# Optimization experiments

Measured on AMD Instinct MI355X. Metric: run time of the kernel, lower is better.

The kernel has to match this reference:

```python
import jax, jax.numpy as jnp
import numpy as np

E = 800_000      # number of edges
D = 256          # d_model_edge
N = 50_000       # number of atoms/nodes


def setup_inputs() -> dict:
    key = jax.random.key(0)
    k1, k2, k3, k4, k5 = jax.random.split(key, 5)
    forces = jax.random.normal(k1, (E, D), dtype=jnp.float32)
    V_st = jax.random.normal(k2, (E, 3), dtype=jnp.float32)
    # MLP([D, D, 1]): Linear(D,D) + act + Linear(D,1). Scaled init for stability.
    W1 = jax.random.normal(k3, (D, D), dtype=jnp.float32) * (1.0 / np.sqrt(D))
    b1 = jnp.zeros((D,), dtype=jnp.float32)
    W2 = jax.random.normal(k4, (D, 1), dtype=jnp.float32) * (1.0 / np.sqrt(D))
    b2 = jnp.zeros((1,), dtype=jnp.float32)
    idx_t = jax.random.randint(k5, (E,), 0, N, dtype=jnp.int64 if jax.config.jax_enable_x64 else jnp.int32)
    return {
        "forces": forces,
        "V_st": V_st,
        "W1": W1,
        "b1": b1,
        "W2": W2,
        "b2": b2,
        "idx_t": idx_t,
        "n_atoms": N,
    }


def reference(forces, V_st, W1, b1, W2, b2, idx_t, n_atoms):
    # out_mlp: Linear(D,D) -> SiLU -> Linear(D,1)
    h = jax.nn.silu(forces @ W1 + b1)          # [E, D]
    s = h @ W2 + b2                            # [E, 1] per-edge scalar
    ev = s * V_st                              # [E, 3] scaled direction vectors
    # scatter-sum over target node indices (reduction='sum')
    out = jax.ops.segment_sum(ev, idx_t, num_segments=n_atoms)  # [N, 3]
    return out
```

## Files before the change

### kernel.cpp

```cpp
#include <hip/hip_runtime.h>
#include <hip/hip_bf16.h>

typedef __attribute__((ext_vector_type(8))) short short8;
typedef __attribute__((ext_vector_type(4))) float floatx4;
typedef unsigned short u16;

#define D 256
#define BM 32
#define NT 128

__device__ __forceinline__ short f2bf(float f) {
    return __builtin_bit_cast(short, __float2bfloat16(f));
}

__global__ void prep_kernel(const float* __restrict__ W1, u16* __restrict__ W1F,
                            float* __restrict__ out, int outn) {
    const int b = blockIdx.x;
    if (b < D) {
        const int k = b, n = threadIdx.x;
        const int k0t = k >> 5, g = (k >> 3) & 3, j = k & 7;
        const int nt = n >> 4, l15 = n & 15;
        W1F[(long)((((k0t << 4) + nt) << 6) + (g << 4) + l15) * 8 + j] = (u16)f2bf(W1[k * D + n]);
    } else {
        int i = (b - D) * 256 + threadIdx.x;
        const int stride = (gridDim.x - D) * 256;
        for (; i < outn; i += stride) out[i] = 0.f;
    }
}

struct R8 { floatx4 f0, f1; };

__launch_bounds__(NT, 4)
__global__ void head_kernel(const float* __restrict__ forces,
                            const float* __restrict__ V_st,
                            const u16*   __restrict__ W1F,
                            const float* __restrict__ b1,
                            const float* __restrict__ W2,
                            const float* __restrict__ b2,
                            const int*   __restrict__ idx_t,
                            float* __restrict__ out,
                            int E) {
    __shared__ u16 Albs[16 * 512];
    __shared__ float s_red[2][BM];

    const int tid  = threadIdx.x;
    const int lane = tid & 63;
    const int wn   = tid >> 6;
    const int l15  = lane & 15;
    const int g    = lane >> 4;

    const long row0 = (long)blockIdx.x * BM;

    float vx = 0.f, vy = 0.f, vz = 0.f;
    int node = -1;
    if (tid < BM) {
        long e = row0 + tid;
        vx = V_st[e * 3 + 0]; vy = V_st[e * 3 + 1]; vz = V_st[e * 3 + 2];
        node = idx_t[e];
    }

    const int arow = tid >> 2;
    const int agg  = tid & 3;
    const float* abase = forces + (row0 + arow) * D + agg * 8;

    R8 r[8];
#pragma unroll
    for (int k0t = 0; k0t < 8; ++k0t) {
        r[k0t].f0 = *(const floatx4*)(abase + k0t * 32);
        r[k0t].f1 = *(const floatx4*)(abase + k0t * 32 + 4);
    }
    const int aslot = ((agg << 4) | (arow & 15)) * 8;
    const int art   = arow >> 4;
#pragma unroll
    for (int k0t = 0; k0t < 8; ++k0t) {
        short8 a;
#pragma unroll
        for (int j = 0; j < 4; ++j) { a[j] = f2bf(r[k0t].f0[j]); a[4 + j] = f2bf(r[k0t].f1[j]); }
        *(short8*)&Albs[(k0t * 2 + art) * 512 + aslot] = a;
    }
    __syncthreads();

    floatx4 acc[2][8];
#pragma unroll
    for (int mr = 0; mr < 2; ++mr)
#pragma unroll
        for (int nc = 0; nc < 8; ++nc)
            acc[mr][nc] = (floatx4){0.f, 0.f, 0.f, 0.f};

#pragma unroll
    for (int k0t = 0; k0t < 8; ++k0t) {
        short8 bf[8], af[2];
#pragma unroll
        for (int nc = 0; nc < 8; ++nc)
            bf[nc] = *(const short8*)(W1F + (long)((k0t * 16 + wn * 8 + nc) * 64 + lane) * 8);
#pragma unroll
        for (int mr = 0; mr < 2; ++mr)
            af[mr] = *(const short8*)&Albs[(k0t * 2 + mr) * 512 + lane * 8];
#pragma unroll
        for (int mr = 0; mr < 2; ++mr)
#pragma unroll
            for (int nc = 0; nc < 8; ++nc)
                acc[mr][nc] = __builtin_amdgcn_mfma_f32_16x16x32_bf16(
                    af[mr], bf[nc], acc[mr][nc], 0, 0, 0);
    }

    float b1v[8], w2v[8];
#pragma unroll
    for (int nc = 0; nc < 8; ++nc) {
        int n = wn * 128 + nc * 16 + l15;
        b1v[nc] = b1[n];
        w2v[nc] = W2[n];
    }
    float part[2][4];
#pragma unroll
    for (int mr = 0; mr < 2; ++mr)
#pragma unroll
        for (int rr = 0; rr < 4; ++rr) {
            float sv = 0.f;
#pragma unroll
            for (int nc = 0; nc < 8; ++nc) {
                float z = acc[mr][nc][rr] + b1v[nc];
                float h = z / (1.f + __expf(-z));
                sv += h * w2v[nc];
            }
            part[mr][rr] = sv;
        }

#pragma unroll
    for (int off = 1; off < 16; off <<= 1)
#pragma unroll
        for (int mr = 0; mr < 2; ++mr)
#pragma unroll
            for (int rr = 0; rr < 4; ++rr)
                part[mr][rr] += __shfl_xor(part[mr][rr], off, 16);

    if (l15 == 0) {
#pragma unroll
        for (int mr = 0; mr < 2; ++mr)
#pragma unroll
            for (int rr = 0; rr < 4; ++rr)
                s_red[wn][mr * 16 + g * 4 + rr] = part[mr][rr];
    }
    __syncthreads();

    if (node >= 0) {
        float sv = s_red[0][tid] + s_red[1][tid] + b2[0];
        atomicAdd(&out[(long)node * 3 + 0], sv * vx);
        atomicAdd(&out[(long)node * 3 + 1], sv * vy);
        atomicAdd(&out[(long)node * 3 + 2], sv * vz);
    }
}

extern "C" void kernel_launch(void* const* d_in, const int* in_sizes, int n_in,
                              void* d_out, int out_size, void* d_ws, size_t ws_size,
                              hipStream_t stream) {
    const float* forces = (const float*)d_in[0];
    const float* V_st   = (const float*)d_in[1];
    const float* W1     = (const float*)d_in[2];
    const float* b1     = (const float*)d_in[3];
    const float* W2     = (const float*)d_in[4];
    const float* b2     = (const float*)d_in[5];
    const int*   idx    = (const int*)d_in[6];
    const int E = in_sizes[6];

    u16* W1F = (u16*)d_ws;

    prep_kernel<<<D + 128, 256, 0, stream>>>(W1, W1F, (float*)d_out, out_size);
    const int grid = E / BM;
    head_kernel<<<grid, NT, 0, stream>>>(forces, V_st, W1F, b1, W2, b2, idx,
                                         (float*)d_out, E);
}
```

Before: 291.3 us.

## Warp-specialize head kernel into persistent producer/consumer with double-buffered LDS

Replaces the one-tile-per-block launch with 512 persistent blocks of 512 threads. Four producer waves load and convert the next 64-row forces tile into a second LDS buffer while four consumer waves run MFMA, SiLU and the W2 reduction on the current tile. The aim is to overlap global-memory streaming of forces with the matrix compute and to cut per-block launch overhead. In exchange, half the waves do no math, a block-wide barrier runs every iteration, and occupancy depends on the larger LDS footprint and the 512-thread launch bounds.

```diff
diff --git a/kernel.cpp b/kernel.cpp
--- a/kernel.cpp
+++ b/kernel.cpp
@@ -6,8 +6,9 @@
 typedef unsigned short u16;
 
 #define D 256
-#define BM 32
-#define NT 128
+#define BM 64
+#define NT 512
+#define NBLK 512
 
 __device__ __forceinline__ short f2bf(float f) {
     return __builtin_bit_cast(short, __float2bfloat16(f));
@@ -28,8 +29,6 @@
     }
 }
 
-struct R8 { floatx4 f0, f1; };
-
 __launch_bounds__(NT, 4)
 __global__ void head_kernel(const float* __restrict__ forces,
                             const float* __restrict__ V_st,
@@ -40,114 +39,121 @@
                             const int*   __restrict__ idx_t,
                             float* __restrict__ out,
                             int E) {
-    __shared__ u16 Albs[16 * 512];
-    __shared__ float s_red[2][BM];
+    __shared__ u16 Abuf[2][32 * 512];
+    __shared__ float s_red[2][2][BM];
 
     const int tid  = threadIdx.x;
     const int lane = tid & 63;
-    const int wn   = tid >> 6;
-    const int l15  = lane & 15;
-    const int g    = lane >> 4;
+    const int w    = tid >> 6;
+    const int ntiles = E / BM;
+    const long b = blockIdx.x;
+    const int niter = (int)((ntiles - b + NBLK - 1) / NBLK);
 
-    const long row0 = (long)blockIdx.x * BM;
+    const int arow  = tid >> 2;
+    const int agg   = tid & 3;
+    const int art   = arow >> 4;
+    const int aslot = ((agg << 4) | (arow & 15)) * 8;
+
+    auto FILL = [&](int buf, long tile) {
+        const float* abase = forces + (tile * BM + arow) * (long)D + agg * 8;
+        floatx4 f0[8], f1[8];
+#pragma unroll
+        for (int k0t = 0; k0t < 8; ++k0t) {
+            f0[k0t] = *(const floatx4*)(abase + k0t * 32);
+            f1[k0t] = *(const floatx4*)(abase + k0t * 32 + 4);
+        }
+#pragma unroll
+        for (int k0t = 0; k0t < 8; ++k0t) {
+            short8 a;
+#pragma unroll
+            for (int j = 0; j < 4; ++j) { a[j] = f2bf(f0[k0t][j]); a[4 + j] = f2bf(f1[k0t][j]); }
+            *(short8*)&Abuf[buf][(k0t * 4 + art) * 512 + aslot] = a;
+        }
+    };
+
+    const int cw  = w - 4;
+    const int wm  = (cw >> 1) & 1;
+    const int wn  = cw & 1;
+    const int l15 = lane & 15;
+    const int g   = lane >> 4;
+
+    if (w < 4) FILL(0, b);
+    __syncthreads();
 
     float vx = 0.f, vy = 0.f, vz = 0.f;
-    int node = -1;
-    if (tid < BM) {
-        long e = row0 + tid;
-        vx = V_st[e * 3 + 0]; vy = V_st[e * 3 + 1]; vz = V_st[e * 3 + 2];
-        node = idx_t[e];
-    }
+    int nd = 0;
 
-    const int arow = tid >> 2;
-    const int agg  = tid & 3;
-    const float* abase = forces + (row0 + arow) * D + agg * 8;
+    for (int i = 0; i < niter; ++i) {
+        const int cur = i & 1;
+        const long t = b + (long)i * NBLK;
 
-    R8 r[8];
+        if (w < 4) {
+            if (i + 1 < niter) FILL(cur ^ 1, t + NBLK);
+        } else {
+            if (w == 4) {
+                long e = t * BM + lane;
+                vx = V_st[e * 3 + 0]; vy = V_st[e * 3 + 1]; vz = V_st[e * 3 + 2];
+                nd = idx_t[e];
+            }
+            floatx4 acc[2][8];
 #pragma unroll
-    for (int k0t = 0; k0t < 8; ++k0t) {
-        r[k0t].f0 = *(const floatx4*)(abase + k0t * 32);
-        r[k0t].f1 = *(const floatx4*)(abase + k0t * 32 + 4);
-    }
-    const int aslot = ((agg << 4) | (arow & 15)) * 8;
-    const int art   = arow >> 4;
+            for (int mr = 0; mr < 2; ++mr)
 #pragma unroll
-    for (int k0t = 0; k0t < 8; ++k0t) {
-        short8 a;
-#pragma unroll
-        for (int j = 0; j < 4; ++j) { a[j] = f2bf(r[k0t].f0[j]); a[4 + j] = f2bf(r[k0t].f1[j]); }
-        *(short8*)&Albs[(k0t * 2 + art) * 512 + aslot] = a;
-    }
-    __syncthreads();
-
-    floatx4 acc[2][8];
-#pragma unroll
-    for (int mr = 0; mr < 2; ++mr)
-#pragma unroll
-        for (int nc = 0; nc < 8; ++nc)
-            acc[mr][nc] = (floatx4){0.f, 0.f, 0.f, 0.f};
+                for (int nc = 0; nc < 8; ++nc)
+                    acc[mr][nc] = (floatx4){0.f, 0.f, 0.f, 0.f};
 
 #pragma unroll
-    for (int k0t = 0; k0t < 8; ++k0t) {
-        short8 bf[8], af[2];
+            for (int k0t = 0; k0t < 8; ++k0t) {
+                short8 af0 = *(const short8*)&Abuf[cur][(k0t * 4 + wm * 2 + 0) * 512 + lane * 8];
+                short8 af1 = *(const short8*)&Abuf[cur][(k0t * 4 + wm * 2 + 1) * 512 + lane * 8];
 #pragma unroll
-        for (int nc = 0; nc < 8; ++nc)
-            bf[nc] = *(const short8*)(W1F + (long)((k0t * 16 + wn * 8 + nc) * 64 + lane) * 8);
+                for (int nc = 0; nc < 8; ++nc) {
+                    short8 bf = *(const short8*)(W1F +
+                        (long)((k0t * 16 + wn * 8 + nc) * 64 + lane) * 8);
+                    acc[0][nc] = __builtin_amdgcn_mfma_f32_16x16x32_bf16(af0, bf, acc[0][nc], 0, 0, 0);
+                    acc[1][nc] = __builtin_amdgcn_mfma_f32_16x16x32_bf16(af1, bf, acc[1][nc], 0, 0, 0);
+                }
+            }
+
+            float part[2][4];
 #pragma unroll
-        for (int mr = 0; mr < 2; ++mr)
-            af[mr] = *(const short8*)&Albs[(k0t * 2 + mr) * 512 + lane * 8];
+            for (int mr = 0; mr < 2; ++mr)
 #pragma unroll
-        for (int mr = 0; mr < 2; ++mr)
+                for (int rr = 0; rr < 4; ++rr) {
+                    float sv = 0.f;
 #pragma unroll
-            for (int nc = 0; nc < 8; ++nc)
-                acc[mr][nc] = __builtin_amdgcn_mfma_f32_16x16x32_bf16(
-                    af[mr], bf[nc], acc[mr][nc], 0, 0, 0);
-    }
-
-    float b1v[8], w2v[8];
+                    for (int nc = 0; nc < 8; ++nc) {
+                        int n = wn * 128 + nc * 16 + l15;
+                        float z = acc[mr][nc][rr] + b1[n];
+                        float h = z / (1.f + __expf(-z));
+                        sv += h * W2[n];
+                    }
+                    part[mr][rr] = sv;
+                }
 #pragma unroll
-    for (int nc = 0; nc < 8; ++nc) {
-        int n = wn * 128 + nc * 16 + l15;
-        b1v[nc] = b1[n];
-        w2v[nc] = W2[n];
-    }
-    float part[2][4];
+            for (int off = 1; off < 16; off <<= 1)
 #pragma unroll
-    for (int mr = 0; mr < 2; ++mr)
+                for (int mr = 0; mr < 2; ++mr)
 #pragma unroll
-        for (int rr = 0; rr < 4; ++rr) {
-            float sv = 0.f;
+                    for (int rr = 0; rr < 4; ++rr)
+                        part[mr][rr] += __shfl_xor(part[mr][rr], off, 16);
+            if (l15 == 0) {
 #pragma unroll
-            for (int nc = 0; nc < 8; ++nc) {
-                float z = acc[mr][nc][rr] + b1v[nc];
-                float h = z / (1.f + __expf(-z));
-                sv += h * w2v[nc];
+                for (int mr = 0; mr < 2; ++mr)
+#pragma unroll
+                    for (int rr = 0; rr < 4; ++rr)
+                        s_red[cur][wn][wm * 32 + mr * 16 + g * 4 + rr] = part[mr][rr];
             }
-            part[mr][rr] = sv;
         }
 
-#pragma unroll
-    for (int off = 1; off < 16; off <<= 1)
-#pragma unroll
-        for (int mr = 0; mr < 2; ++mr)
-#pragma unroll
-            for (int rr = 0; rr < 4; ++rr)
-                part[mr][rr] += __shfl_xor(part[mr][rr], off, 16);
+        __syncthreads();
 
-    if (l15 == 0) {
-#pragma unroll
-        for (int mr = 0; mr < 2; ++mr)
-#pragma unroll
-            for (int rr = 0; rr < 4; ++rr)
-                s_red[wn][mr * 16 + g * 4 + rr] = part[mr][rr];
-    }
-    __syncthreads();
-
-    if (node >= 0) {
-        float sv = s_red[0][tid] + s_red[1][tid] + b2[0];
-        atomicAdd(&out[(long)node * 3 + 0], sv * vx);
-        atomicAdd(&out[(long)node * 3 + 1], sv * vy);
-        atomicAdd(&out[(long)node * 3 + 2], sv * vz);
+        if (w == 4) {
+            float sv = s_red[cur][0][lane] + s_red[cur][1][lane] + b2[0];
+            atomicAdd(&out[(long)nd * 3 + 0], sv * vx);
+            atomicAdd(&out[(long)nd * 3 + 1], sv * vy);
+            atomicAdd(&out[(long)nd * 3 + 2], sv * vz);
+        }
     }
 }
 
@@ -166,7 +172,6 @@
     u16* W1F = (u16*)d_ws;
 
     prep_kernel<<<D + 128, 256, 0, stream>>>(W1, W1F, (float*)d_out, out_size);
-    const int grid = E / BM;
-    head_kernel<<<grid, NT, 0, stream>>>(forces, V_st, W1F, b1, W2, b2, idx,
+    head_kernel<<<NBLK, NT, 0, stream>>>(forces, V_st, W1F, b1, W2, b2, idx,
                                          (float*)d_out, E);
 }
```

Measured after the change: 778.0 us. +167.1%, slower.

## Double row tile to 64 edges with four waves splitting the output columns

Applied to the files above, without the earlier changes.

Each block now processes 64 edges with 256 threads, and each of four waves computes a 64x64 column slice instead of two waves computing 32x128. This halves the W1 fragment loads per MFMA per wave and amortizes the weight traffic over more rows per block. In exchange, the LDS footprint per block grows and the cross-wave reduction now sums four partials instead of two, with fewer blocks in the grid.

```diff
diff --git a/kernel.cpp b/kernel.cpp
--- a/kernel.cpp
+++ b/kernel.cpp
@@ -6,8 +6,8 @@
 typedef unsigned short u16;
 
 #define D 256
-#define BM 32
-#define NT 128
+#define BM 64
+#define NT 256
 
 __device__ __forceinline__ short f2bf(float f) {
     return __builtin_bit_cast(short, __float2bfloat16(f));
@@ -40,12 +40,12 @@
                             const int*   __restrict__ idx_t,
                             float* __restrict__ out,
                             int E) {
-    __shared__ u16 Albs[16 * 512];
-    __shared__ float s_red[2][BM];
+    __shared__ u16 Albs[32 * 512];
+    __shared__ float s_red[4][BM];
 
     const int tid  = threadIdx.x;
     const int lane = tid & 63;
-    const int wn   = tid >> 6;
+    const int wq   = tid >> 6;
     const int l15  = lane & 15;
     const int g    = lane >> 4;
 
@@ -76,75 +76,75 @@
         short8 a;
 #pragma unroll
         for (int j = 0; j < 4; ++j) { a[j] = f2bf(r[k0t].f0[j]); a[4 + j] = f2bf(r[k0t].f1[j]); }
-        *(short8*)&Albs[(k0t * 2 + art) * 512 + aslot] = a;
+        *(short8*)&Albs[(k0t * 4 + art) * 512 + aslot] = a;
     }
     __syncthreads();
 
-    floatx4 acc[2][8];
+    floatx4 acc[4][4];
 #pragma unroll
-    for (int mr = 0; mr < 2; ++mr)
+    for (int rt = 0; rt < 4; ++rt)
 #pragma unroll
-        for (int nc = 0; nc < 8; ++nc)
-            acc[mr][nc] = (floatx4){0.f, 0.f, 0.f, 0.f};
+        for (int nc = 0; nc < 4; ++nc)
+            acc[rt][nc] = (floatx4){0.f, 0.f, 0.f, 0.f};
 
 #pragma unroll
     for (int k0t = 0; k0t < 8; ++k0t) {
-        short8 bf[8], af[2];
+        short8 bf[4], af[4];
 #pragma unroll
-        for (int nc = 0; nc < 8; ++nc)
-            bf[nc] = *(const short8*)(W1F + (long)((k0t * 16 + wn * 8 + nc) * 64 + lane) * 8);
+        for (int nc = 0; nc < 4; ++nc)
+            bf[nc] = *(const short8*)(W1F + (long)((k0t * 16 + wq * 4 + nc) * 64 + lane) * 8);
 #pragma unroll
-        for (int mr = 0; mr < 2; ++mr)
-            af[mr] = *(const short8*)&Albs[(k0t * 2 + mr) * 512 + lane * 8];
+        for (int rt = 0; rt < 4; ++rt)
+            af[rt] = *(const short8*)&Albs[(k0t * 4 + rt) * 512 + lane * 8];
 #pragma unroll
-        for (int mr = 0; mr < 2; ++mr)
+        for (int rt = 0; rt < 4; ++rt)
 #pragma unroll
-            for (int nc = 0; nc < 8; ++nc)
-                acc[mr][nc] = __builtin_amdgcn_mfma_f32_16x16x32_bf16(
-                    af[mr], bf[nc], acc[mr][nc], 0, 0, 0);
+            for (int nc = 0; nc < 4; ++nc)
+                acc[rt][nc] = __builtin_amdgcn_mfma_f32_16x16x32_bf16(
+                    af[rt], bf[nc], acc[rt][nc], 0, 0, 0);
     }
 
-    float b1v[8], w2v[8];
+    float b1v[4], w2v[4];
 #pragma unroll
-    for (int nc = 0; nc < 8; ++nc) {
-        int n = wn * 128 + nc * 16 + l15;
+    for (int nc = 0; nc < 4; ++nc) {
+        int n = wq * 64 + nc * 16 + l15;
         b1v[nc] = b1[n];
         w2v[nc] = W2[n];
     }
-    float part[2][4];
+    float part[4][4];
 #pragma unroll
-    for (int mr = 0; mr < 2; ++mr)
+    for (int rt = 0; rt < 4; ++rt)
 #pragma unroll
         for (int rr = 0; rr < 4; ++rr) {
             float sv = 0.f;
 #pragma unroll
-            for (int nc = 0; nc < 8; ++nc) {
-                float z = acc[mr][nc][rr] + b1v[nc];
+            for (int nc = 0; nc < 4; ++nc) {
+                float z = acc[rt][nc][rr] + b1v[nc];
                 float h = z / (1.f + __expf(-z));
                 sv += h * w2v[nc];
             }
-            part[mr][rr] = sv;
+            part[rt][rr] = sv;
         }
 
 #pragma unroll
     for (int off = 1; off < 16; off <<= 1)
 #pragma unroll
-        for (int mr = 0; mr < 2; ++mr)
+        for (int rt = 0; rt < 4; ++rt)
 #pragma unroll
             for (int rr = 0; rr < 4; ++rr)
-                part[mr][rr] += __shfl_xor(part[mr][rr], off, 16);
+                part[rt][rr] += __shfl_xor(part[rt][rr], off, 16);
 
     if (l15 == 0) {
 #pragma unroll
-        for (int mr = 0; mr < 2; ++mr)
+        for (int rt = 0; rt < 4; ++rt)
 #pragma unroll
             for (int rr = 0; rr < 4; ++rr)
-                s_red[wn][mr * 16 + g * 4 + rr] = part[mr][rr];
+                s_red[wq][rt * 16 + g * 4 + rr] = part[rt][rr];
     }
     __syncthreads();
 
     if (node >= 0) {
-        float sv = s_red[0][tid] + s_red[1][tid] + b2[0];
+        float sv = s_red[0][tid] + s_red[1][tid] + s_red[2][tid] + s_red[3][tid] + b2[0];
         atomicAdd(&out[(long)node * 3 + 0], sv * vx);
         atomicAdd(&out[(long)node * 3 + 1], sv * vy);
         atomicAdd(&out[(long)node * 3 + 2], sv * vz);
```

Measured after the change: 280.4 us, median of 2. 3.7% less time.
